# Kernel optimization log

Measured on AMD Instinct MI355X. Metric: run time of the kernel, lower is better.

The kernel has to match this reference:

```python
import jax, jax.numpy as jnp
import numpy as np

N = 20000; E = 320000; IN = 128; OUT = 128; H = 8; D = 16
SQRT_DK = float(D) ** 0.5

def setup_inputs() -> dict:
    key = jax.random.key(0)
    ks = jax.random.split(key, 20)
    s = 0.05
    glorot = (6.0 / (D + D)) ** 0.5
    inp = dict(
        h_a=jax.random.normal(ks[0], (N, IN), jnp.float32),
        h_b=jax.random.normal(ks[1], (N, IN), jnp.float32),
        Wk=jax.random.normal(ks[2], (2, IN, OUT), jnp.float32) * s,
        bk=jnp.zeros((2, OUT), jnp.float32),
        Wq=jax.random.normal(ks[3], (2, IN, OUT), jnp.float32) * s,
        bq=jnp.zeros((2, OUT), jnp.float32),
        Wv=jax.random.normal(ks[4], (2, IN, OUT), jnp.float32) * s,
        bv=jnp.zeros((2, OUT), jnp.float32),
        Wa=jax.random.normal(ks[5], (2, OUT, OUT), jnp.float32) * s,
        ba=jnp.zeros((2, OUT), jnp.float32),
        rel_att=jax.random.normal(ks[6], (4, H, D, D), jnp.float32) * glorot,
        rel_msg=jax.random.normal(ks[7], (4, H, D, D), jnp.float32) * glorot,
        rel_pri=jnp.ones((4, H), jnp.float32),
        skip=jnp.ones((2,), jnp.float32),
    )
    names = ["src_aa", "dst_aa", "src_ab", "dst_ab", "src_ba", "dst_ba", "src_bb", "dst_bb"]
    for i, name in enumerate(names):
        inp[name] = jax.random.randint(ks[8 + i], (E,), 0, N, jnp.int32)
    return inp

def _relation(h_src, h_dst, src, dst, Wk_t, bk_t, Wq_t, bq_t, Wv_t, bv_t, att, msg, pri):
    # relation-specific K/V transform + Q projection
    k = (h_src @ Wk_t + bk_t).reshape(-1, H, D)
    v = (h_src @ Wv_t + bv_t).reshape(-1, H, D)
    q = (h_dst @ Wq_t + bq_t).reshape(-1, H, D)
    k = jnp.einsum('nhd,hde->nhe', k, att)
    v = jnp.einsum('nhd,hde->nhe', v, msg)
    # edge dot-product score (v_dot_u: q[dst] . k[src]), [E, H]
    score = jnp.einsum('ehd,ehd->eh', q[dst], k[src]) * pri / SQRT_DK
    # edge softmax normalized by dst
    smax = jax.ops.segment_max(score, dst, num_segments=N)
    ex = jnp.exp(score - smax[dst])
    ssum = jax.ops.segment_sum(ex, dst, num_segments=N)
    attn = ex / ssum[dst]
    # weighted scatter-aggregate, [N, H, D]
    return jax.ops.segment_sum(v[src] * attn[:, :, None], dst, num_segments=N)

def reference(h_a, h_b, Wk, bk, Wq, bq, Wv, bv, Wa, ba, rel_att, rel_msg, rel_pri, skip,
              src_aa, dst_aa, src_ab, dst_ab, src_ba, dst_ba, src_bb, dst_bb):
    agg_aa = _relation(h_a, h_a, src_aa, dst_aa, Wk[0], bk[0], Wq[0], bq[0], Wv[0], bv[0], rel_att[0], rel_msg[0], rel_pri[0])
    agg_ab = _relation(h_a, h_b, src_ab, dst_ab, Wk[0], bk[0], Wq[1], bq[1], Wv[0], bv[0], rel_att[1], rel_msg[1], rel_pri[1])
    agg_ba = _relation(h_b, h_a, src_ba, dst_ba, Wk[1], bk[1], Wq[0], bq[0], Wv[1], bv[1], rel_att[2], rel_msg[2], rel_pri[2])
    agg_bb = _relation(h_b, h_b, src_bb, dst_bb, Wk[1], bk[1], Wq[1], bq[1], Wv[1], bv[1], rel_att[3], rel_msg[3], rel_pri[3])
    # cross_reducer='mean' over the 2 relations targeting each node type
    t_a = (0.5 * (agg_aa + agg_ba)).reshape(N, OUT)
    t_b = (0.5 * (agg_ab + agg_bb)).reshape(N, OUT)
    al_a = jax.nn.sigmoid(skip[0])
    al_b = jax.nn.sigmoid(skip[1])
    new_a = al_a * (t_a @ Wa[0] + ba[0]) + (1.0 - al_a) * h_a
    new_b = al_b * (t_b @ Wa[1] + ba[1]) + (1.0 - al_b) * h_b
    return new_a, new_b
```

## Files before the change

kernel.cpp:

```cpp
#include <hip/hip_runtime.h>
#include <stdint.h>

#define N_NODES 20000
#define N_EDGES 320000
#define C 128
#define H 8
#define D 16
#define SLOT 64
#define NRANGE 5000
#define BUCKETS 2500
#define BCAP 224

#define P_CVT 2500
#define P_ZERO 157
#define P_PACK 128
#define P_FUSE 32
#define PB_EDGES 16384
#define PART_BLOCKS 80
#define PROJ_BLOCKS 3130
#define MB_TOTAL (PART_BLOCKS + PROJ_BLOCKS)

typedef short s16x8 __attribute__((ext_vector_type(8)));
typedef float f32x4 __attribute__((ext_vector_type(4)));

__device__ __forceinline__ unsigned short f2bf(float f) {
    unsigned int b = __float_as_uint(f);
    b += 0x7fffu + ((b >> 16) & 1u);
    return (unsigned short)(b >> 16);
}
__device__ __forceinline__ float bf2f(unsigned int u) {
    return __uint_as_float(u << 16);
}
__device__ __forceinline__ float bf_lo(unsigned int u) {
    return __uint_as_float(u << 16);
}
__device__ __forceinline__ float bf_hi(unsigned int u) {
    return __uint_as_float(u & 0xffff0000u);
}

__global__ __launch_bounds__(256) void prep_k(const float* __restrict__ h_a, const float* __restrict__ h_b,
                                              unsigned short* __restrict__ oa, unsigned short* __restrict__ ob,
                                              const float* __restrict__ Wq, const float* __restrict__ Wa,
                                              unsigned short* __restrict__ Wqt, unsigned short* __restrict__ Wat,
                                              const float* __restrict__ Wk, const float* __restrict__ Wv,
                                              const float* __restrict__ bk, const float* __restrict__ bv,
                                              const float* __restrict__ att, const float* __restrict__ msg,
                                              unsigned short* __restrict__ Wkt, unsigned short* __restrict__ Wvt,
                                              float* __restrict__ bkt, float* __restrict__ bvt,
                                              int* __restrict__ cur) {
    __shared__ float sa[D * D], sm[D * D];
    int bid = blockIdx.x;
    int tid = threadIdx.x;
    if (bid < P_CVT) {
        int i = (bid * 256 + tid) * 4;
        float4 va = *(const float4*)(h_a + i);
        float4 vb = *(const float4*)(h_b + i);
        ushort4 ua = { f2bf(va.x), f2bf(va.y), f2bf(va.z), f2bf(va.w) };
        ushort4 ub = { f2bf(vb.x), f2bf(vb.y), f2bf(vb.z), f2bf(vb.w) };
        *(ushort4*)(oa + i) = ua;
        *(ushort4*)(ob + i) = ub;
        return;
    }
    bid -= P_CVT;
    if (bid < P_ZERO) {
        int i = bid * 256 + tid;
        if (i < 40000) ((int4*)cur)[i] = make_int4(0, 0, 0, 0);
        return;
    }
    bid -= P_ZERO;
    if (bid < P_PACK) {
        int n = bid;
        int t = tid >> 7, i = tid & 127;
        Wqt[(t * C + n) * C + i] = f2bf(Wq[(t * C + i) * C + n]);
        Wat[(t * C + n) * C + i] = f2bf(Wa[(t * C + i) * C + n]);
        return;
    }
    bid -= P_PACK;
    {
        int r = bid >> 3, h = bid & 7;
        int t = r >> 1;
        if (tid < D * D) {
            sa[tid] = att[(r * H + h) * D * D + tid];
            sm[tid] = msg[(r * H + h) * D * D + tid];
        }
        __syncthreads();
        int i = tid & 127;
        for (int e = (tid >> 7); e < D; e += 2) {
            float sk = 0.f, sv = 0.f;
            for (int d = 0; d < D; ++d) {
                sk += Wk[(t * C + i) * C + h * D + d] * sa[d * D + e];
                sv += Wv[(t * C + i) * C + h * D + d] * sm[d * D + e];
            }
            Wkt[(r * C + h * D + e) * C + i] = f2bf(sk);
            Wvt[(r * C + h * D + e) * C + i] = f2bf(sv);
        }
        if (tid < D) {
            int e = tid;
            float sk = 0.f, sv = 0.f;
            for (int d = 0; d < D; ++d) {
                sk += bk[t * C + h * D + d] * sa[d * D + e];
                sv += bv[t * C + h * D + d] * sm[d * D + e];
            }
            bkt[r * C + h * D + e] = sk;
            bvt[r * C + h * D + e] = sv;
        }
    }
}

__global__ __launch_bounds__(256) void mega_k(const int* __restrict__ s0, const int* __restrict__ s1,
                                              const int* __restrict__ s2, const int* __restrict__ s3,
                                              const int* __restrict__ d0, const int* __restrict__ d1,
                                              const int* __restrict__ d2, const int* __restrict__ d3,
                                              int* __restrict__ cur, unsigned int* __restrict__ part,
                                              const unsigned short* __restrict__ ha,
                                              const unsigned short* __restrict__ hb,
                                              const unsigned short* __restrict__ Wqt,
                                              const unsigned short* __restrict__ Wkt,
                                              const unsigned short* __restrict__ Wvt,
                                              const float* __restrict__ bq,
                                              const float* __restrict__ bkt,
                                              const float* __restrict__ bvt,
                                              unsigned short* __restrict__ Qa,
                                              unsigned short* __restrict__ Qb,
                                              unsigned short* __restrict__ Kall,
                                              unsigned short* __restrict__ Vall) {
    __shared__ int hcnt[BUCKETS];
    __shared__ int hbase[BUCKETS];
    int bid = blockIdx.x;
    int tid = threadIdx.x;

    if (bid < PART_BLOCKS) {
        int r  = bid & 3;
        int pb = bid >> 2;
        int start = pb * PB_EDGES;
        int nval = N_EDGES - start;
        if (nval > PB_EDGES) nval = PB_EDGES;
        int nq = nval >> 2;
        const int* dd = (r == 0) ? d0 : (r == 1) ? d1 : (r == 2) ? d2 : d3;
        const int* ss = (r == 0) ? s0 : (r == 1) ? s1 : (r == 2) ? s2 : s3;
        for (int b = tid; b < BUCKETS; b += 256) hcnt[b] = 0;
        __syncthreads();
        for (int i = tid; i < nq; i += 256) {
            int4 d4 = *(const int4*)(dd + start + i * 4);
            atomicAdd(&hcnt[d4.x >> 3], 1);
            atomicAdd(&hcnt[d4.y >> 3], 1);
            atomicAdd(&hcnt[d4.z >> 3], 1);
            atomicAdd(&hcnt[d4.w >> 3], 1);
        }
        __syncthreads();
        for (int b = tid; b < BUCKETS; b += 256) {
            int c = hcnt[b];
            hbase[b] = c ? atomicAdd(&cur[(r * BUCKETS + b) * 16], c) : 0;
            hcnt[b] = 0;
        }
        __syncthreads();
        for (int i = tid; i < nq; i += 256) {
            int4 d4 = *(const int4*)(dd + start + i * 4);
            int4 s4 = *(const int4*)(ss + start + i * 4);
            int b0 = d4.x >> 3, b1 = d4.y >> 3, b2 = d4.z >> 3, b3 = d4.w >> 3;
            int i0 = atomicAdd(&hcnt[b0], 1);
            int i1 = atomicAdd(&hcnt[b1], 1);
            int i2 = atomicAdd(&hcnt[b2], 1);
            int i3 = atomicAdd(&hcnt[b3], 1);
            int p0 = hbase[b0] + i0, p1 = hbase[b1] + i1, p2 = hbase[b2] + i2, p3 = hbase[b3] + i3;
            if (p0 < BCAP) part[(size_t)(r * BUCKETS + b0) * BCAP + p0] = (unsigned int)s4.x | ((unsigned int)(d4.x & 7) << 15);
            if (p1 < BCAP) part[(size_t)(r * BUCKETS + b1) * BCAP + p1] = (unsigned int)s4.y | ((unsigned int)(d4.y & 7) << 15);
            if (p2 < BCAP) part[(size_t)(r * BUCKETS + b2) * BCAP + p2] = (unsigned int)s4.z | ((unsigned int)(d4.z & 7) << 15);
            if (p3 < BCAP) part[(size_t)(r * BUCKETS + b3) * BCAP + p3] = (unsigned int)s4.w | ((unsigned int)(d4.w & 7) << 15);
        }
        return;
    }
    int proj_id = bid - PART_BLOCKS;
    int j = proj_id / 313;
    int xb = proj_id - j * 313;
    const unsigned short* A;
    const unsigned short* Wt;
    const float* bias;
    unsigned short* Out;
    if (j < 2) {
        A = j ? hb : ha; Wt = Wqt + j * C * C; bias = bq + j * C; Out = j ? Qb : Qa;
    } else if (j < 6) {
        int r = j - 2;
        A = (r < 2) ? ha : hb; Wt = Wkt + r * C * C; bias = bkt + r * C;
        Out = Kall + (size_t)r * N_NODES * C;
    } else {
        int r = j - 6;
        A = (r < 2) ? ha : hb; Wt = Wvt + r * C * C; bias = bvt + r * C;
        Out = Vall + (size_t)r * N_NODES * C;
    }
    int wid = threadIdx.x >> 6, l = threadIdx.x & 63;
    int row_base = xb * 64 + wid * 16;
    int lm = l & 15, q = l >> 4;
    f32x4 acc[8] = {};
    int arow = row_base + lm;
    if (arow >= N_NODES) arow = N_NODES - 1;
    const s16x8* Ap = (const s16x8*)(A + (size_t)arow * C);
#pragma unroll
    for (int kc = 0; kc < 4; ++kc) {
        s16x8 af = Ap[kc * 4 + q];
#pragma unroll
        for (int t = 0; t < 8; ++t) {
            s16x8 bf = *(const s16x8*)(Wt + (t * 16 + lm) * C + kc * 32 + q * 8);
            acc[t] = __builtin_amdgcn_mfma_f32_16x16x32_bf16(af, bf, acc[t], 0, 0, 0);
        }
    }
#pragma unroll
    for (int t = 0; t < 8; ++t) {
        int col = t * 16 + lm;
        float b = bias[col];
#pragma unroll
        for (int i = 0; i < 4; ++i) {
            int row = row_base + q * 4 + i;
            if (row < N_NODES) Out[(size_t)row * C + col] = f2bf(acc[t][i] + b);
        }
    }
}

__global__ __launch_bounds__(256) void final_mm(const unsigned short* __restrict__ AggAll,
                                                const unsigned short* __restrict__ WatAll,
                                                const float* __restrict__ baAll,
                                                const float* __restrict__ skip,
                                                const float* __restrict__ h_a,
                                                const float* __restrict__ h_b,
                                                float* __restrict__ OutAll) {
    int ty = blockIdx.y;
    const unsigned short* Agg = AggAll + (size_t)ty * N_NODES * C;
    const unsigned short* Wat = WatAll + ty * C * C;
    const float* ba = baAll + ty * C;
    const float* h_orig = ty ? h_b : h_a;
    float* Out = OutAll + (size_t)ty * N_NODES * C;
    int wid = threadIdx.x >> 6, l = threadIdx.x & 63;
    int row_base = blockIdx.x * 64 + wid * 16;
    int lm = l & 15, q = l >> 4;
    f32x4 acc[8] = {};
    int arow = row_base + lm;
    if (arow >= N_NODES) arow = N_NODES - 1;
    const s16x8* Ap = (const s16x8*)(Agg + (size_t)arow * C);
#pragma unroll
    for (int kc = 0; kc < 4; ++kc) {
        s16x8 af = Ap[kc * 4 + q];
#pragma unroll
        for (int t = 0; t < 8; ++t) {
            s16x8 bf = *(const s16x8*)(Wat + (t * 16 + lm) * C + kc * 32 + q * 8);
            acc[t] = __builtin_amdgcn_mfma_f32_16x16x32_bf16(af, bf, acc[t], 0, 0, 0);
        }
    }
    float al = 1.f / (1.f + __expf(-skip[ty]));
#pragma unroll
    for (int t = 0; t < 8; ++t) {
        int col = t * 16 + lm;
        float b = ba[col];
#pragma unroll
        for (int i = 0; i < 4; ++i) {
            int row = row_base + q * 4 + i;
            if (row < N_NODES)
                Out[(size_t)row * C + col] = al * (acc[t][i] + b) + (1.f - al) * h_orig[(size_t)row * C + col];
        }
    }
}

__global__ __launch_bounds__(256) void node_p2(const int* __restrict__ cur,
                                               const unsigned int* __restrict__ part,
                                               const unsigned int* __restrict__ Kall,
                                               const unsigned int* __restrict__ Vall,
                                               const float* __restrict__ pri,
                                               const unsigned int* __restrict__ Qa,
                                               const unsigned int* __restrict__ Qb,
                                               unsigned int* __restrict__ agg) {
    __shared__ unsigned short slot[2][4][SLOT];
    __shared__ int cnt[2][4];
    int g = blockIdx.x;
    int type = (g >= NRANGE) ? 1 : 0;
    int range = g - type * NRANGE;
    int relA = type ? 1 : 0;
    int relB = type ? 3 : 2;
    if (threadIdx.x < 8) ((int*)cnt)[threadIdx.x] = 0;
    __syncthreads();
    int bkt = range >> 1;
    int w   = range & 1;
#pragma unroll
    for (int rr = 0; rr < 2; ++rr) {
        int rel = rr ? relB : relA;
        int c = cur[(rel * BUCKETS + bkt) * 16];
        if (c > BCAP) c = BCAP;
        const unsigned int* pp = part + (size_t)(rel * BUCKETS + bkt) * BCAP;
        for (int i = threadIdx.x; i < c; i += 256) {
            unsigned int rec = pp[i];
            int dlow = (rec >> 15) & 7;
            if ((dlow >> 2) == w) {
                int dof = dlow & 3;
                int p = atomicAdd(&cnt[rr][dof], 1);
                if (p < SLOT) slot[rr][dof][p] = (unsigned short)(rec & 0x7fffu);
            }
        }
    }
    __syncthreads();

    int wid = threadIdx.x >> 6, l = threadIdx.x & 63;
    int eg = l >> 4;
    int j  = l & 15;
    int hg = j >> 1;
    int dof = wid;
    int n = range * 4 + dof;
    const unsigned int* Q32 = type ? Qb : Qa;
    uint4 qv = *(const uint4*)(Q32 + (size_t)n * 64 + j * 4);
    float q0 = bf_lo(qv.x), q1 = bf_hi(qv.x), q2 = bf_lo(qv.y), q3 = bf_hi(qv.y);
    float q4 = bf_lo(qv.z), q5 = bf_hi(qv.z), q6 = bf_lo(qv.w), q7 = bf_hi(qv.w);
    float out[8] = {};

#pragma unroll 1
    for (int rr = 0; rr < 2; ++rr) {
        int rel = rr ? relB : relA;
        const char* Kb = (const char*)(Kall + (size_t)rel * N_NODES * 64);
        const char* Vb = (const char*)(Vall + (size_t)rel * N_NODES * 64);
        float pv = pri[rel * 8 + hg] * 0.25f;
        int deg = cnt[rr][dof];
        if (deg > SLOT) deg = SLOT;
        float m = -1e30f, sum = 0.f;
        float acc[8] = {};
        for (int base = 0; base < deg; base += 16) {
            float s[4];
            uint4 vv[4];
#pragma unroll
            for (int i = 0; i < 4; ++i) {
                int idx = base + i * 4 + eg;
                float d = -1e30f;
                uint4 v = {0u, 0u, 0u, 0u};
                if (idx < deg) {
                    unsigned off = ((unsigned)slot[rr][dof][idx] << 8) | ((unsigned)j << 4);
                    uint4 kv = *(const uint4*)(Kb + off);
                    v = *(const uint4*)(Vb + off);
                    d = q0 * bf_lo(kv.x) + q1 * bf_hi(kv.x)
                      + q2 * bf_lo(kv.y) + q3 * bf_hi(kv.y)
                      + q4 * bf_lo(kv.z) + q5 * bf_hi(kv.z)
                      + q6 * bf_lo(kv.w) + q7 * bf_hi(kv.w);
                    d += __shfl_xor(d, 1);
                    d *= pv;
                }
                s[i] = d;
                vv[i] = v;
            }
            float mloc = fmaxf(fmaxf(s[0], s[1]), fmaxf(s[2], s[3]));
            float mnew = fmaxf(m, mloc);
            float alpha = __expf(m - mnew);
            sum *= alpha;
#pragma unroll
            for (int c2 = 0; c2 < 8; ++c2) acc[c2] *= alpha;
            m = mnew;
#pragma unroll
            for (int i = 0; i < 4; ++i) {
                float ww = (s[i] > -1e29f) ? __expf(s[i] - m) : 0.f;
                sum += ww;
                acc[0] += ww * bf_lo(vv[i].x); acc[1] += ww * bf_hi(vv[i].x);
                acc[2] += ww * bf_lo(vv[i].y); acc[3] += ww * bf_hi(vv[i].y);
                acc[4] += ww * bf_lo(vv[i].z); acc[5] += ww * bf_hi(vv[i].z);
                acc[6] += ww * bf_lo(vv[i].w); acc[7] += ww * bf_hi(vv[i].w);
            }
        }
        float m1 = fmaxf(m, __shfl_xor(m, 16));
        float m2 = fmaxf(m1, __shfl_xor(m1, 32));
        float beta = __expf(m - m2);
        sum *= beta;
        sum += __shfl_xor(sum, 16);
        sum += __shfl_xor(sum, 32);
#pragma unroll
        for (int c2 = 0; c2 < 8; ++c2) {
            float a = acc[c2] * beta;
            a += __shfl_xor(a, 16);
            a += __shfl_xor(a, 32);
            acc[c2] = a;
        }
        if (deg > 0) {
            float rs = 1.f / sum;
#pragma unroll
            for (int c2 = 0; c2 < 8; ++c2) out[c2] += acc[c2] * rs;
        }
    }
    if (eg == 0) {
        uint4 pk;
        pk.x = (unsigned int)f2bf(0.5f * out[0]) | ((unsigned int)f2bf(0.5f * out[1]) << 16);
        pk.y = (unsigned int)f2bf(0.5f * out[2]) | ((unsigned int)f2bf(0.5f * out[3]) << 16);
        pk.z = (unsigned int)f2bf(0.5f * out[4]) | ((unsigned int)f2bf(0.5f * out[5]) << 16);
        pk.w = (unsigned int)f2bf(0.5f * out[6]) | ((unsigned int)f2bf(0.5f * out[7]) << 16);
        *(uint4*)(agg + ((size_t)type * N_NODES + n) * 64 + j * 4) = pk;
    }
}

extern "C" void kernel_launch(void* const* d_in, const int* in_sizes, int n_in,
                              void* d_out, int out_size, void* d_ws, size_t ws_size,
                              hipStream_t stream) {
    const float* h_a  = (const float*)d_in[0];
    const float* h_b  = (const float*)d_in[1];
    const float* Wk   = (const float*)d_in[2];
    const float* bk   = (const float*)d_in[3];
    const float* Wq   = (const float*)d_in[4];
    const float* bq   = (const float*)d_in[5];
    const float* Wv   = (const float*)d_in[6];
    const float* bv   = (const float*)d_in[7];
    const float* Wa   = (const float*)d_in[8];
    const float* ba   = (const float*)d_in[9];
    const float* att  = (const float*)d_in[10];
    const float* msg  = (const float*)d_in[11];
    const float* pri  = (const float*)d_in[12];
    const float* skip = (const float*)d_in[13];
    const int* srcs[4] = {(const int*)d_in[14], (const int*)d_in[16], (const int*)d_in[18], (const int*)d_in[20]};
    const int* dsts[4] = {(const int*)d_in[15], (const int*)d_in[17], (const int*)d_in[19], (const int*)d_in[21]};
    float* out = (float*)d_out;

    char* w = (char*)d_ws;
    auto alloc = [&](size_t bytes) {
        char* p = w;
        w += (bytes + 255) & ~(size_t)255;
        return p;
    };
    unsigned short* ha_bf = (unsigned short*)alloc((size_t)N_NODES * C * 2);
    unsigned short* hb_bf = (unsigned short*)alloc((size_t)N_NODES * C * 2);
    unsigned short* Qa    = (unsigned short*)alloc((size_t)N_NODES * C * 2);
    unsigned short* Qb    = (unsigned short*)alloc((size_t)N_NODES * C * 2);
    unsigned short* Kall  = (unsigned short*)alloc((size_t)4 * N_NODES * C * 2);
    unsigned short* Vall  = (unsigned short*)alloc((size_t)4 * N_NODES * C * 2);
    unsigned short* Wqt   = (unsigned short*)alloc(2 * C * C * 2);
    unsigned short* Wat   = (unsigned short*)alloc(2 * C * C * 2);
    unsigned short* Wkt   = (unsigned short*)alloc(4 * C * C * 2);
    unsigned short* Wvt   = (unsigned short*)alloc(4 * C * C * 2);
    float* bkt            = (float*)alloc(4 * C * 4);
    float* bvt            = (float*)alloc(4 * C * 4);
    int* cur              = (int*)alloc((size_t)4 * BUCKETS * 16 * 4);
    unsigned int* part    = (unsigned int*)alloc((size_t)4 * BUCKETS * BCAP * 4);
    unsigned short* agg   = (unsigned short*)alloc((size_t)2 * N_NODES * C * 2);

    prep_k<<<P_CVT + P_ZERO + P_PACK + P_FUSE, 256, 0, stream>>>(
        h_a, h_b, ha_bf, hb_bf, Wq, Wa, Wqt, Wat,
        Wk, Wv, bk, bv, att, msg, Wkt, Wvt, bkt, bvt, cur);

    mega_k<<<MB_TOTAL, 256, 0, stream>>>(
        srcs[0], srcs[1], srcs[2], srcs[3],
        dsts[0], dsts[1], dsts[2], dsts[3],
        cur, part,
        ha_bf, hb_bf, Wqt, Wkt, Wvt, bq, bkt, bvt,
        Qa, Qb, Kall, Vall);

    node_p2<<<2 * NRANGE, 256, 0, stream>>>(cur, part,
                                            (const unsigned int*)Kall, (const unsigned int*)Vall,
                                            pri,
                                            (const unsigned int*)Qa, (const unsigned int*)Qb,
                                            (unsigned int*)agg);

    final_mm<<<dim3(313, 2), 256, 0, stream>>>(agg, Wat, ba, skip, h_a, h_b, out);
}
```

Baseline: 310.8 us.

## Fuse output projection into node aggregation kernel and pack float math

Drops the separate final_mm kernel: each node_p2 block stages its 4 aggregated node rows in shared memory, then computes the Wa projection, bias, sigmoid skip blend and fp32 output directly with scalar packed-float dot products. This removes the bf16 agg buffer round trip and one kernel launch. The inner score and value accumulation loops are also rewritten with 2-wide float vectors to encourage packed FMA instructions. In exchange, the MFMA matmul becomes per-thread scalar work that reads Wa rows from global or cache in every block. It also adds a block-wide barrier and shared memory to the aggregation kernel.

```diff
diff --git a/kernel.cpp b/kernel.cpp
--- a/kernel.cpp
+++ b/kernel.cpp
@@ -22,6 +22,7 @@
 
 typedef short s16x8 __attribute__((ext_vector_type(8)));
 typedef float f32x4 __attribute__((ext_vector_type(4)));
+typedef float f32x2 __attribute__((ext_vector_type(2)));
 
 __device__ __forceinline__ unsigned short f2bf(float f) {
     unsigned int b = __float_as_uint(f);
@@ -36,6 +37,9 @@
 }
 __device__ __forceinline__ float bf_hi(unsigned int u) {
     return __uint_as_float(u & 0xffff0000u);
+}
+__device__ __forceinline__ f32x2 bfpair(unsigned int u) {
+    f32x2 r; r.x = bf_lo(u); r.y = bf_hi(u); return r;
 }
 
 __global__ __launch_bounds__(256) void prep_k(const float* __restrict__ h_a, const float* __restrict__ h_b,
@@ -216,49 +220,6 @@
     }
 }
 
-__global__ __launch_bounds__(256) void final_mm(const unsigned short* __restrict__ AggAll,
-                                                const unsigned short* __restrict__ WatAll,
-                                                const float* __restrict__ baAll,
-                                                const float* __restrict__ skip,
-                                                const float* __restrict__ h_a,
-                                                const float* __restrict__ h_b,
-                                                float* __restrict__ OutAll) {
-    int ty = blockIdx.y;
-    const unsigned short* Agg = AggAll + (size_t)ty * N_NODES * C;
-    const unsigned short* Wat = WatAll + ty * C * C;
-    const float* ba = baAll + ty * C;
-    const float* h_orig = ty ? h_b : h_a;
-    float* Out = OutAll + (size_t)ty * N_NODES * C;
-    int wid = threadIdx.x >> 6, l = threadIdx.x & 63;
-    int row_base = blockIdx.x * 64 + wid * 16;
-    int lm = l & 15, q = l >> 4;
-    f32x4 acc[8] = {};
-    int arow = row_base + lm;
-    if (arow >= N_NODES) arow = N_NODES - 1;
-    const s16x8* Ap = (const s16x8*)(Agg + (size_t)arow * C);
-#pragma unroll
-    for (int kc = 0; kc < 4; ++kc) {
-        s16x8 af = Ap[kc * 4 + q];
-#pragma unroll
-        for (int t = 0; t < 8; ++t) {
-            s16x8 bf = *(const s16x8*)(Wat + (t * 16 + lm) * C + kc * 32 + q * 8);
-            acc[t] = __builtin_amdgcn_mfma_f32_16x16x32_bf16(af, bf, acc[t], 0, 0, 0);
-        }
-    }
-    float al = 1.f / (1.f + __expf(-skip[ty]));
-#pragma unroll
-    for (int t = 0; t < 8; ++t) {
-        int col = t * 16 + lm;
-        float b = ba[col];
-#pragma unroll
-        for (int i = 0; i < 4; ++i) {
-            int row = row_base + q * 4 + i;
-            if (row < N_NODES)
-                Out[(size_t)row * C + col] = al * (acc[t][i] + b) + (1.f - al) * h_orig[(size_t)row * C + col];
-        }
-    }
-}
-
 __global__ __launch_bounds__(256) void node_p2(const int* __restrict__ cur,
                                                const unsigned int* __restrict__ part,
                                                const unsigned int* __restrict__ Kall,
@@ -266,9 +227,15 @@
                                                const float* __restrict__ pri,
                                                const unsigned int* __restrict__ Qa,
                                                const unsigned int* __restrict__ Qb,
-                                               unsigned int* __restrict__ agg) {
+                                               const unsigned short* __restrict__ WatAll,
+                                               const float* __restrict__ baAll,
+                                               const float* __restrict__ skip,
+                                               const float* __restrict__ h_a,
+                                               const float* __restrict__ h_b,
+                                               float* __restrict__ OutAll) {
     __shared__ unsigned short slot[2][4][SLOT];
     __shared__ int cnt[2][4];
+    __shared__ __align__(16) float aggl[4][C];
     int g = blockIdx.x;
     int type = (g >= NRANGE) ? 1 : 0;
     int range = g - type * NRANGE;
@@ -304,9 +271,9 @@
     int n = range * 4 + dof;
     const unsigned int* Q32 = type ? Qb : Qa;
     uint4 qv = *(const uint4*)(Q32 + (size_t)n * 64 + j * 4);
-    float q0 = bf_lo(qv.x), q1 = bf_hi(qv.x), q2 = bf_lo(qv.y), q3 = bf_hi(qv.y);
-    float q4 = bf_lo(qv.z), q5 = bf_hi(qv.z), q6 = bf_lo(qv.w), q7 = bf_hi(qv.w);
-    float out[8] = {};
+    f32x2 q2[4];
+    q2[0] = bfpair(qv.x); q2[1] = bfpair(qv.y); q2[2] = bfpair(qv.z); q2[3] = bfpair(qv.w);
+    float out8[8] = {};
 
 #pragma unroll 1
     for (int rr = 0; rr < 2; ++rr) {
@@ -317,7 +284,7 @@
         int deg = cnt[rr][dof];
         if (deg > SLOT) deg = SLOT;
         float m = -1e30f, sum = 0.f;
-        float acc[8] = {};
+        f32x2 acc2[4] = {};
         for (int base = 0; base < deg; base += 16) {
             float s[4];
             uint4 vv[4];
@@ -330,10 +297,11 @@
                     unsigned off = ((unsigned)slot[rr][dof][idx] << 8) | ((unsigned)j << 4);
                     uint4 kv = *(const uint4*)(Kb + off);
                     v = *(const uint4*)(Vb + off);
-                    d = q0 * bf_lo(kv.x) + q1 * bf_hi(kv.x)
-                      + q2 * bf_lo(kv.y) + q3 * bf_hi(kv.y)
-                      + q4 * bf_lo(kv.z) + q5 * bf_hi(kv.z)
-                      + q6 * bf_lo(kv.w) + q7 * bf_hi(kv.w);
+                    f32x2 d2 = q2[0] * bfpair(kv.x);
+                    d2 += q2[1] * bfpair(kv.y);
+                    d2 += q2[2] * bfpair(kv.z);
+                    d2 += q2[3] * bfpair(kv.w);
+                    d = d2.x + d2.y;
                     d += __shfl_xor(d, 1);
                     d *= pv;
                 }
@@ -345,16 +313,16 @@
             float alpha = __expf(m - mnew);
             sum *= alpha;
 #pragma unroll
-            for (int c2 = 0; c2 < 8; ++c2) acc[c2] *= alpha;
+            for (int c2 = 0; c2 < 4; ++c2) acc2[c2] *= alpha;
             m = mnew;
 #pragma unroll
             for (int i = 0; i < 4; ++i) {
                 float ww = (s[i] > -1e29f) ? __expf(s[i] - m) : 0.f;
                 sum += ww;
-                acc[0] += ww * bf_lo(vv[i].x); acc[1] += ww * bf_hi(vv[i].x);
-                acc[2] += ww * bf_lo(vv[i].y); acc[3] += ww * bf_hi(vv[i].y);
-                acc[4] += ww * bf_lo(vv[i].z); acc[5] += ww * bf_hi(vv[i].z);
-                acc[6] += ww * bf_lo(vv[i].w); acc[7] += ww * bf_hi(vv[i].w);
+                acc2[0] += bfpair(vv[i].x) * ww;
+                acc2[1] += bfpair(vv[i].y) * ww;
+                acc2[2] += bfpair(vv[i].z) * ww;
+                acc2[3] += bfpair(vv[i].w) * ww;
             }
         }
         float m1 = fmaxf(m, __shfl_xor(m, 16));
@@ -363,26 +331,50 @@
         sum *= beta;
         sum += __shfl_xor(sum, 16);
         sum += __shfl_xor(sum, 32);
-#pragma unroll
-        for (int c2 = 0; c2 < 8; ++c2) {
-            float a = acc[c2] * beta;
-            a += __shfl_xor(a, 16);
-            a += __shfl_xor(a, 32);
-            acc[c2] = a;
-        }
-        if (deg > 0) {
-            float rs = 1.f / sum;
-#pragma unroll
-            for (int c2 = 0; c2 < 8; ++c2) out[c2] += acc[c2] * rs;
+        float rs = (deg > 0) ? 0.f : 0.f;
+        rs = (deg > 0) ? 1.f / sum : 0.f;
+#pragma unroll
+        for (int c2 = 0; c2 < 4; ++c2) {
+            float ax = acc2[c2].x * beta;
+            float ay = acc2[c2].y * beta;
+            ax += __shfl_xor(ax, 16); ax += __shfl_xor(ax, 32);
+            ay += __shfl_xor(ay, 16); ay += __shfl_xor(ay, 32);
+            out8[2 * c2]     += ax * rs;
+            out8[2 * c2 + 1] += ay * rs;
         }
     }
     if (eg == 0) {
-        uint4 pk;
-        pk.x = (unsigned int)f2bf(0.5f * out[0]) | ((unsigned int)f2bf(0.5f * out[1]) << 16);
-        pk.y = (unsigned int)f2bf(0.5f * out[2]) | ((unsigned int)f2bf(0.5f * out[3]) << 16);
-        pk.z = (unsigned int)f2bf(0.5f * out[4]) | ((unsigned int)f2bf(0.5f * out[5]) << 16);
-        pk.w = (unsigned int)f2bf(0.5f * out[6]) | ((unsigned int)f2bf(0.5f * out[7]) << 16);
-        *(uint4*)(agg + ((size_t)type * N_NODES + n) * 64 + j * 4) = pk;
+#pragma unroll
+        for (int c2 = 0; c2 < 8; ++c2) aggl[dof][j * 8 + c2] = 0.5f * out8[c2];
+    }
+    __syncthreads();
+    const unsigned short* Wt = WatAll + type * C * C;
+    const float* bat = baAll + type * C;
+    const float* horig = type ? h_b : h_a;
+    float* Outp = OutAll + (size_t)type * N_NODES * C;
+    float al = 1.f / (1.f + __expf(-skip[type]));
+#pragma unroll
+    for (int it = 0; it < 2; ++it) {
+        int e = it * 256 + threadIdx.x;
+        int nd = e >> 7, col = e & 127;
+        int node = range * 4 + nd;
+        const uint4* wr = (const uint4*)(Wt + (size_t)col * C);
+        const float4* ag4 = (const float4*)aggl[nd];
+        f32x2 a2 = {};
+#pragma unroll
+        for (int kc = 0; kc < 16; ++kc) {
+            uint4 wv = wr[kc];
+            float4 av0 = ag4[kc * 2];
+            float4 av1 = ag4[kc * 2 + 1];
+            f32x2 p;
+            p.x = av0.x; p.y = av0.y; a2 += p * bfpair(wv.x);
+            p.x = av0.z; p.y = av0.w; a2 += p * bfpair(wv.y);
+            p.x = av1.x; p.y = av1.y; a2 += p * bfpair(wv.z);
+            p.x = av1.z; p.y = av1.w; a2 += p * bfpair(wv.w);
+        }
+        float acc = a2.x + a2.y;
+        Outp[(size_t)node * C + col] =
+            al * (acc + bat[col]) + (1.f - al) * horig[(size_t)node * C + col];
     }
 }
 
@@ -427,7 +419,6 @@
     float* bvt            = (float*)alloc(4 * C * 4);
     int* cur              = (int*)alloc((size_t)4 * BUCKETS * 16 * 4);
     unsigned int* part    = (unsigned int*)alloc((size_t)4 * BUCKETS * BCAP * 4);
-    unsigned short* agg   = (unsigned short*)alloc((size_t)2 * N_NODES * C * 2);
 
     prep_k<<<P_CVT + P_ZERO + P_PACK + P_FUSE, 256, 0, stream>>>(
         h_a, h_b, ha_bf, hb_bf, Wq, Wa, Wqt, Wat,
@@ -444,7 +435,5 @@
                                             (const unsigned int*)Kall, (const unsigned int*)Vall,
                                             pri,
                                             (const unsigned int*)Qa, (const unsigned int*)Qb,
-                                            (unsigned int*)agg);
-
-    final_mm<<<dim3(313, 2), 256, 0, stream>>>(agg, Wat, ba, skip, h_a, h_b, out);
-}
+                                            Wat, ba, skip, h_a, h_b, out);
+}
```

New measurement: 578.6 us. +86.1%, slower.
